# Optimization experiments

Measured on AMD Instinct MI355X. Metric: run time of the kernel, lower is better.

Reference implementation:

```python
import jax, jax.numpy as jnp
import numpy as np

N_NODES = 50000
N_EDGES = 1200000
IN_FEATS = 64
OUT_FEATS = 64
NEG_SLOPE = 0.01  # F.leaky_relu default


def setup_inputs() -> dict:
    key = jax.random.key(0)
    k1, k2, k3, k4, k5, k6 = jax.random.split(key, 6)
    feature = jax.random.normal(k1, (N_NODES, IN_FEATS), dtype=jnp.float32)
    attn_w = jax.random.normal(k2, (2 * IN_FEATS, 1), dtype=jnp.float32) * 0.1
    lin_w = jax.random.normal(k3, (OUT_FEATS, 2 * IN_FEATS), dtype=jnp.float32) * 0.1
    lin_b = jax.random.normal(k4, (OUT_FEATS,), dtype=jnp.float32) * 0.1
    src = jax.random.randint(k5, (N_EDGES,), 0, N_NODES, dtype=jnp.int32)
    dst = jax.random.randint(k6, (N_EDGES,), 0, N_NODES, dtype=jnp.int32)
    return {"feature": feature, "attn_w": attn_w, "lin_w": lin_w,
            "lin_b": lin_b, "src": src, "dst": dst}


def reference(feature, attn_w, lin_w, lin_b, src, dst):
    N = feature.shape[0]
    # edge attention: leaky_relu(attn_fc([h_src, h_dst]))
    # split attn weight to avoid materializing the [E, 2*in] concat
    a_src, a_dst = attn_w[:IN_FEATS, 0], attn_w[IN_FEATS:, 0]
    e = jax.nn.leaky_relu(feature[src] @ a_src + feature[dst] @ a_dst,
                          negative_slope=NEG_SLOPE)  # [E]
    # segment softmax over incoming edges of each destination node
    emax = jax.ops.segment_max(e, dst, num_segments=N)
    emax = jnp.where(jnp.isfinite(emax), emax, 0.0)  # guard empty segments
    ex = jnp.exp(e - emax[dst])                       # [E]
    denom = jax.ops.segment_sum(ex, dst, num_segments=N)          # [N]
    num = jax.ops.segment_sum(ex[:, None] * feature[src], dst,
                              num_segments=N)                      # [N, in]
    hm = jnp.where(denom[:, None] > 0, num / denom[:, None], 0.0)
    # node apply: relu(Linear([h, hm]))
    h = jnp.concatenate([feature, hm], axis=1) @ lin_w.T + lin_b
    return jax.nn.relu(h)
```

## Files before the change

### kernel.cpp

```cpp
#include <hip/hip_runtime.h>
#include <math.h>

#define N_NODES 50000
#define N_EDGES 1200000
#define F 64
#define CAP 49
#define OVF_MAX 1024
#define NBIN 782
#define BSTR 16
#define CAP_BIN 2304
#define TILE 8192
#define NTILE ((N_EDGES + TILE - 1) / TILE)

typedef __attribute__((ext_vector_type(8))) short short8;
typedef __attribute__((ext_vector_type(4))) float v4f;


__device__ __forceinline__ unsigned short f32_to_bf16_rne(float f) {
    unsigned u = __float_as_uint(f);
    return (unsigned short)((u + 0x7FFFu + ((u >> 16) & 1u)) >> 16);
}
__device__ __forceinline__ float bf16_to_f32(unsigned short u) {
    return __uint_as_float(((unsigned)u) << 16);
}

__global__ void k_prep(const float* __restrict__ feature,
                       const float* __restrict__ attn_w,
                       float* __restrict__ s, float* __restrict__ dd,
                       int* __restrict__ bin_cnt, int* __restrict__ ovf_cnt,
                       unsigned short* __restrict__ fb) {
    int gid = blockIdx.x * blockDim.x + threadIdx.x;
    if (gid < NBIN * BSTR) bin_cnt[gid] = 0;
    if (gid == NBIN * BSTR) *ovf_cnt = 0;
    int wave = gid >> 6;
    int lane = threadIdx.x & 63;
    if (wave >= N_NODES) return;
    float f = feature[wave * F + lane];
    fb[wave * F + lane] = f32_to_bf16_rne(f);
    float sv = f * attn_w[lane];
    float dv = f * attn_w[F + lane];
    #pragma unroll
    for (int o = 32; o > 0; o >>= 1) {
        sv += __shfl_down(sv, o, 64);
        dv += __shfl_down(dv, o, 64);
    }
    if (lane == 0) {
        s[wave] = sv;
        dd[wave] = dv;
    }
}

__global__ __launch_bounds__(256) void k_bin(
        const int* __restrict__ src, const int* __restrict__ dst,
        int* __restrict__ bin_cnt, unsigned* __restrict__ binned) {
    __shared__ unsigned ord[TILE];
    __shared__ int cnt_l[NBIN], off_l[NBIN], cur_l[NBIN], base_g[NBIN];
    __shared__ int buf[256];
    int t = threadIdx.x;
    int e0 = blockIdx.x * TILE;
    int ecnt = N_EDGES - e0; if (ecnt > TILE) ecnt = TILE;
    for (int i = t; i < NBIN; i += 256) cnt_l[i] = 0;
    __syncthreads();
    int n4 = ecnt >> 2;
    const int4* s4p = (const int4*)src + (e0 >> 2);
    const int4* d4p = (const int4*)dst + (e0 >> 2);
    for (int c = t; c < n4; c += 256) {
        int4 d4 = d4p[c];
        atomicAdd(&cnt_l[d4.x >> 6], 1);
        atomicAdd(&cnt_l[d4.y >> 6], 1);
        atomicAdd(&cnt_l[d4.z >> 6], 1);
        atomicAdd(&cnt_l[d4.w >> 6], 1);
    }
    __syncthreads();
    int c0[4];
    int sum = 0;
    #pragma unroll
    for (int j = 0; j < 4; j++) {
        int idx = t * 4 + j;
        c0[j] = (idx < NBIN) ? cnt_l[idx] : 0;
        sum += c0[j];
    }
    buf[t] = sum;
    __syncthreads();
    #pragma unroll
    for (int d = 1; d < 256; d <<= 1) {
        int x = (t >= d) ? buf[t - d] : 0;
        __syncthreads();
        buf[t] += x;
        __syncthreads();
    }
    int excl = buf[t] - sum;
    #pragma unroll
    for (int j = 0; j < 4; j++) {
        int idx = t * 4 + j;
        if (idx < NBIN) {
            off_l[idx] = excl;
            cur_l[idx] = excl;
            base_g[idx] = atomicAdd(&bin_cnt[idx * BSTR], c0[j]);
        }
        excl += c0[j];
    }
    __syncthreads();
    for (int c = t; c < n4; c += 256) {
        int4 d4 = d4p[c];
        int4 s4 = s4p[c];
        int dv[4] = {d4.x, d4.y, d4.z, d4.w};
        int sv[4] = {s4.x, s4.y, s4.z, s4.w};
        #pragma unroll
        for (int u = 0; u < 4; u++) {
            int r = atomicAdd(&cur_l[dv[u] >> 6], 1);
            ord[r] = (((unsigned)dv[u]) << 16) | (unsigned)sv[u];
        }
    }
    __syncthreads();
    for (int i = t; i < ecnt; i += 256) {
        unsigned v = ord[i];
        int b = v >> 22;
        int pos = base_g[b] + (i - off_l[b]);
        if (pos < CAP_BIN) binned[(size_t)b * CAP_BIN + pos] = v;
    }
}

__global__ __launch_bounds__(256) void k_fused(
        const unsigned* __restrict__ binned, const int* __restrict__ bin_cnt,
        int* __restrict__ cnt, unsigned short* __restrict__ bucket,
        int* __restrict__ ovf_cnt, unsigned* __restrict__ ovf,
        const float* __restrict__ s, const float* __restrict__ dd,
        const unsigned short* __restrict__ fb,
        const float* __restrict__ lin_w, const float* __restrict__ lin_b,
        float* __restrict__ out) {
    __shared__ int cnt_l[64];
    __shared__ unsigned short buck_l[64 * CAP];
    __shared__ unsigned short Wl[64 * 136];
    __shared__ float xl[4][16][64];
    int t = threadIdx.x;
    int wid = t >> 6, lane = t & 63;
    int bin = blockIdx.x;
    int n0 = bin << 6;
    int nn = N_NODES - n0; if (nn > 64) nn = 64;
    for (int i = t; i < 64 * 128; i += 256)
        Wl[(i >> 7) * 136 + (i & 127)] = f32_to_bf16_rne(lin_w[i]);
    if (t < 64) cnt_l[t] = 0;
    __syncthreads();
    int E = bin_cnt[bin * BSTR];
    if (E > CAP_BIN) E = CAP_BIN;
    const unsigned* be = binned + (size_t)bin * CAP_BIN;
    for (int i = t; i < E; i += 256) {
        unsigned v = be[i];
        int local = (v >> 16) & 63;
        int sid = (int)(v & 0xFFFFu);
        int r = atomicAdd(&cnt_l[local], 1);
        if (r < CAP) {
            buck_l[local * CAP + r] = (unsigned short)sid;
        } else {
            int o = atomicAdd(ovf_cnt, 1);
            if (o < OVF_MAX)
                ovf[o] = ((unsigned)(n0 + local) << 16) | (unsigned)sid;
        }
    }
    __syncthreads();
    if (t < nn) {
        cnt[n0 + t] = cnt_l[t];
        if (cnt_l[t] > CAP) {
            for (int k2 = 0; k2 < CAP; k2++)
                bucket[(size_t)(n0 + t) * CAP + k2] = buck_l[t * CAP + k2];
        }
    }
    __syncthreads();
    const ushort4* f4 = (const ushort4*)fb;
    for (int j = 0; j < 16; j++) {
        int local = wid * 16 + j;
        if (local >= nn) break;
        int deg = cnt_l[local];
        if (deg == 0 || deg > CAP) {
            if (lane < 16) {
                v4f z = {0.0f, 0.0f, 0.0f, 0.0f};
                ((v4f*)&xl[wid][j][0])[lane] = z;
            }
            continue;
        }
        int si = 0;
        float ev = -1e30f;
        if (lane < deg) {
            si = (int)buck_l[local * CAP + lane];
            float v = s[si] + dd[n0 + local];
            ev = v > 0.0f ? v : 0.01f * v;
        }
        float m = ev;
        #pragma unroll
        for (int o = 32; o > 0; o >>= 1)
            m = fmaxf(m, __shfl_xor(m, o, 64));
        float p = (lane < deg) ? __expf(ev - m) : 0.0f;
        float l = p;
        #pragma unroll
        for (int o = 32; o > 0; o >>= 1)
            l += __shfl_xor(l, o, 64);
        p *= __builtin_amdgcn_rcpf(l);
        int grp = lane >> 4;
        int c16 = lane & 15;
        ushort4 fv0[8], fv1[8];
        #pragma unroll
        for (int u = 0; u < 8; u++) {
            int sk = __shfl(si, u * 4 + grp, 64);
            fv0[u] = f4[sk * 16 + c16];
        }
        bool two = deg > 32;
        if (two) {
            #pragma unroll
            for (int u = 0; u < 8; u++) {
                int sk = __shfl(si, 32 + u * 4 + grp, 64);
                fv1[u] = f4[sk * 16 + c16];
            }
        }
        float a0 = 0.0f, a1 = 0.0f, a2 = 0.0f, a3 = 0.0f;
        #pragma unroll
        for (int u = 0; u < 8; u++) {
            float pw = __shfl(p, u * 4 + grp, 64);
            a0 = fmaf(pw, bf16_to_f32(fv0[u].x), a0);
            a1 = fmaf(pw, bf16_to_f32(fv0[u].y), a1);
            a2 = fmaf(pw, bf16_to_f32(fv0[u].z), a2);
            a3 = fmaf(pw, bf16_to_f32(fv0[u].w), a3);
        }
        if (two) {
            #pragma unroll
            for (int u = 0; u < 8; u++) {
                float pw = __shfl(p, 32 + u * 4 + grp, 64);
                a0 = fmaf(pw, bf16_to_f32(fv1[u].x), a0);
                a1 = fmaf(pw, bf16_to_f32(fv1[u].y), a1);
                a2 = fmaf(pw, bf16_to_f32(fv1[u].z), a2);
                a3 = fmaf(pw, bf16_to_f32(fv1[u].w), a3);
            }
        }
        a0 += __shfl_xor(a0, 16, 64); a0 += __shfl_xor(a0, 32, 64);
        a1 += __shfl_xor(a1, 16, 64); a1 += __shfl_xor(a1, 32, 64);
        a2 += __shfl_xor(a2, 16, 64); a2 += __shfl_xor(a2, 32, 64);
        a3 += __shfl_xor(a3, 16, 64); a3 += __shfl_xor(a3, 32, 64);
        if (lane < 16) {
            v4f st = {a0, a1, a2, a3};
            ((v4f*)&xl[wid][j][0])[c16] = st;
        }
    }
    int n0w = n0 + wid * 16;
    if (n0w >= N_NODES) return;
    int m = lane & 15, quad = lane >> 4;
    short8 afr[4];
    #pragma unroll
    for (int ks = 0; ks < 2; ks++) {
        int kb = ks * 32 + quad * 8;
        afr[ks] = *(const short8*)&fb[(size_t)(n0w + m) * F + kb];
    }
    #pragma unroll
    for (int ks = 2; ks < 4; ks++) {
        int kb = ks * 32 + quad * 8 - 64;
        const float* sp = &xl[wid][m][kb];
        float4 x0 = ((const float4*)sp)[0];
        float4 x1 = ((const float4*)sp)[1];
        short8 a;
        a[0] = (short)f32_to_bf16_rne(x0.x);
        a[1] = (short)f32_to_bf16_rne(x0.y);
        a[2] = (short)f32_to_bf16_rne(x0.z);
        a[3] = (short)f32_to_bf16_rne(x0.w);
        a[4] = (short)f32_to_bf16_rne(x1.x);
        a[5] = (short)f32_to_bf16_rne(x1.y);
        a[6] = (short)f32_to_bf16_rne(x1.z);
        a[7] = (short)f32_to_bf16_rne(x1.w);
        afr[ks] = a;
    }
    #pragma unroll
    for (int nt = 0; nt < 4; nt++) {
        v4f acc = {0.0f, 0.0f, 0.0f, 0.0f};
        #pragma unroll
        for (int ks = 0; ks < 4; ks++) {
            int kb = ks * 32 + quad * 8;
            short8 b = *(const short8*)&Wl[(nt * 16 + m) * 136 + kb];
            acc = __builtin_amdgcn_mfma_f32_16x16x32_bf16(afr[ks], b, acc,
                                                          0, 0, 0);
        }
        int colo = nt * 16 + m;
        float bias = lin_b[colo];
        #pragma unroll
        for (int r = 0; r < 4; r++) {
            int row = quad * 4 + r;
            float v = acc[r] + bias;
            out[(size_t)(n0w + row) * F + colo] = fmaxf(v, 0.0f);
        }
    }
}

__global__ __launch_bounds__(256) void k_cleanup(
        const unsigned short* __restrict__ bucket,
        const int* __restrict__ cnt,
        const int* __restrict__ ovf_cnt, const unsigned int* __restrict__ ovf,
        const float* __restrict__ s, const float* __restrict__ dd,
        const float* __restrict__ feature,
        const float* __restrict__ lin_w, const float* __restrict__ lin_b,
        float* __restrict__ out) {
    int M = *ovf_cnt;
    if (M > OVF_MAX) M = OVF_MAX;
    if (M == 0) return;
    __shared__ float Wl[64 * 129];
    __shared__ int list[128];
    __shared__ int nlist;
    __shared__ unsigned short edg[4][256];
    __shared__ float xc[4][128];
    int t = threadIdx.x;
    for (int i = t; i < 64 * 128; i += 256)
        Wl[(i >> 7) * 129 + (i & 127)] = lin_w[i];
    if (t == 0) {
        nlist = 0;
        for (int i = 0; i < M; i++) {
            int d = (int)(ovf[i] >> 16);
            bool seen = false;
            for (int j = 0; j < nlist; j++) if (list[j] == d) seen = true;
            if (!seen && nlist < 128) list[nlist++] = d;
        }
    }
    __syncthreads();
    int wid = t >> 6, lane = t & 63;
    for (int idx = wid; idx < nlist; idx += 4) {
        int n = list[idx];
        int deg = cnt[n];
        if (lane < CAP) edg[wid][lane] = bucket[n * CAP + lane];
        int k2 = CAP;
        for (int base = 0; base < M; base += 64) {
            int i2 = base + lane;
            unsigned val = 0;
            bool mt = false;
            if (i2 < M) { val = ovf[i2]; mt = ((int)(val >> 16) == n); }
            unsigned long long mask = __ballot(mt);
            if (mt) {
                int pos = k2 + __popcll(mask & ((1ULL << lane) - 1ULL));
                if (pos < 256) edg[wid][pos] = (unsigned short)(val & 0xFFFFu);
            }
            k2 += __popcll(mask);
        }
        __threadfence_block();
        int nd = deg < 256 ? deg : 256;
        float m = -1e30f, l = 0.0f, acc = 0.0f;
        float dn = dd[n];
        for (int c0 = 0; c0 < nd; c0 += 64) {
            int j = c0 + lane;
            int sid = 0;
            float ev = -1e30f;
            if (j < nd) {
                sid = (int)edg[wid][j];
                float v = s[sid] + dn;
                ev = v > 0.0f ? v : 0.01f * v;
            }
            float cm = ev;
            #pragma unroll
            for (int o = 32; o > 0; o >>= 1)
                cm = fmaxf(cm, __shfl_xor(cm, o, 64));
            float np = (j < nd) ? __expf(ev - cm) : 0.0f;
            float cl = np;
            #pragma unroll
            for (int o = 32; o > 0; o >>= 1)
                cl += __shfl_xor(cl, o, 64);
            float cacc = 0.0f;
            int c = nd - c0; if (c > 64) c = 64;
            for (int k = 0; k < c; k += 16) {
                float fvv[16];
                #pragma unroll
                for (int u = 0; u < 16; u++) {
                    int sk = __builtin_amdgcn_readlane(sid, k + u);
                    fvv[u] = feature[sk * F + lane];
                }
                #pragma unroll
                for (int u = 0; u < 16; u++) {
                    float pk = __uint_as_float(
                        __builtin_amdgcn_readlane(__float_as_uint(np), k + u));
                    cacc = fmaf(pk, fvv[u], cacc);
                }
            }
            float mn = fmaxf(m, cm);
            float sc = __expf(m - mn);
            float sc2 = __expf(cm - mn);
            l = l * sc + cl * sc2;
            acc = acc * sc + cacc * sc2;
            m = mn;
        }
        float hm = acc / l;
        xc[wid][lane] = feature[n * F + lane];
        xc[wid][64 + lane] = hm;
        __threadfence_block();
        float oa = lin_b[lane];
        #pragma unroll
        for (int k = 0; k < 128; k++)
            oa += xc[wid][k] * Wl[lane * 129 + k];
        out[n * F + lane] = fmaxf(oa, 0.0f);
    }
}

extern "C" void kernel_launch(void* const* d_in, const int* in_sizes, int n_in,
                              void* d_out, int out_size, void* d_ws, size_t ws_size,
                              hipStream_t stream) {
    const float* feature = (const float*)d_in[0];
    const float* attn_w  = (const float*)d_in[1];
    const float* lin_w   = (const float*)d_in[2];
    const float* lin_b   = (const float*)d_in[3];
    const int*   src     = (const int*)d_in[4];
    const int*   dst     = (const int*)d_in[5];
    float* out = (float*)d_out;
    char* ws = (char*)d_ws;

    float*          s       = (float*)(ws);
    float*          dd      = (float*)(ws + 200000);
    int*            cnt     = (int*)  (ws + 400000);
    int*            bin_cnt = (int*)  (ws + 600000);
    int*            ovf_cnt = (int*)  (ws + 650048);
    unsigned*       ovf     = (unsigned*)(ws + 650112);
    unsigned short* bucket  = (unsigned short*)(ws + 654208);
    unsigned*       binned  = (unsigned*)(ws + 5554208);
    unsigned short* fb      = (unsigned short*)(ws + 12761120);

    k_prep<<<(N_NODES * 64) / 256, 256, 0, stream>>>(
        feature, attn_w, s, dd, bin_cnt, ovf_cnt, fb);
    k_bin<<<NTILE, 256, 0, stream>>>(src, dst, bin_cnt, binned);
    k_fused<<<NBIN, 256, 0, stream>>>(
        binned, bin_cnt, cnt, bucket, ovf_cnt, ovf, s, dd, fb,
        lin_w, lin_b, out);
    k_cleanup<<<1, 256, 0, stream>>>(
        bucket, cnt, ovf_cnt, ovf, s, dd, feature, lin_w, lin_b, out);
}
```

Before: 143.1 us.

## Cache packed edges in registers during binning and shrink fused-kernel LDS with bf16 staging

In the binning kernel, each thread now loads src/dst once into a 32-entry register array of packed (dst<<16|src) words and reuses them for the scatter pass, instead of reading global memory twice. In the fused kernel, the aggregated-neighbor staging buffer is stored as bf16 with a padded stride rather than fp32, and launch bounds request 4 blocks per SM. The smaller staging buffer cuts LDS use, which can allow more resident blocks, and the MFMA A-fragment load becomes a direct short8 read. The per-thread register array in k_bin raises register pressure, and bf16 rounding now happens before the LDS store rather than after the read, which should give the same values.

```diff
diff --git a/kernel.cpp b/kernel.cpp
--- a/kernel.cpp
+++ b/kernel.cpp
@@ -11,6 +11,7 @@
 #define CAP_BIN 2304
 #define TILE 8192
 #define NTILE ((N_EDGES + TILE - 1) / TILE)
+#define XSTR 72
 
 typedef __attribute__((ext_vector_type(8))) short short8;
 typedef __attribute__((ext_vector_type(4))) float v4f;
@@ -64,12 +65,24 @@
     int n4 = ecnt >> 2;
     const int4* s4p = (const int4*)src + (e0 >> 2);
     const int4* d4p = (const int4*)dst + (e0 >> 2);
-    for (int c = t; c < n4; c += 256) {
-        int4 d4 = d4p[c];
-        atomicAdd(&cnt_l[d4.x >> 6], 1);
-        atomicAdd(&cnt_l[d4.y >> 6], 1);
-        atomicAdd(&cnt_l[d4.z >> 6], 1);
-        atomicAdd(&cnt_l[d4.w >> 6], 1);
+    unsigned pk[32];
+    int ng = 0;
+    #pragma unroll
+    for (int k = 0; k < 8; k++) {
+        int c = t + k * 256;
+        if (c < n4) {
+            int4 d4 = d4p[c];
+            int4 s4 = s4p[c];
+            pk[4 * k + 0] = (((unsigned)d4.x) << 16) | (unsigned)s4.x;
+            pk[4 * k + 1] = (((unsigned)d4.y) << 16) | (unsigned)s4.y;
+            pk[4 * k + 2] = (((unsigned)d4.z) << 16) | (unsigned)s4.z;
+            pk[4 * k + 3] = (((unsigned)d4.w) << 16) | (unsigned)s4.w;
+            atomicAdd(&cnt_l[pk[4 * k + 0] >> 22], 1);
+            atomicAdd(&cnt_l[pk[4 * k + 1] >> 22], 1);
+            atomicAdd(&cnt_l[pk[4 * k + 2] >> 22], 1);
+            atomicAdd(&cnt_l[pk[4 * k + 3] >> 22], 1);
+            ng = k + 1;
+        }
     }
     __syncthreads();
     int c0[4];
@@ -101,15 +114,12 @@
         excl += c0[j];
     }
     __syncthreads();
-    for (int c = t; c < n4; c += 256) {
-        int4 d4 = d4p[c];
-        int4 s4 = s4p[c];
-        int dv[4] = {d4.x, d4.y, d4.z, d4.w};
-        int sv[4] = {s4.x, s4.y, s4.z, s4.w};
+    for (int k = 0; k < ng; k++) {
         #pragma unroll
         for (int u = 0; u < 4; u++) {
-            int r = atomicAdd(&cur_l[dv[u] >> 6], 1);
-            ord[r] = (((unsigned)dv[u]) << 16) | (unsigned)sv[u];
+            unsigned v = pk[4 * k + u];
+            int r = atomicAdd(&cur_l[v >> 22], 1);
+            ord[r] = v;
         }
     }
     __syncthreads();
@@ -121,7 +131,7 @@
     }
 }
 
-__global__ __launch_bounds__(256) void k_fused(
+__global__ __launch_bounds__(256, 4) void k_fused(
         const unsigned* __restrict__ binned, const int* __restrict__ bin_cnt,
         int* __restrict__ cnt, unsigned short* __restrict__ bucket,
         int* __restrict__ ovf_cnt, unsigned* __restrict__ ovf,
@@ -132,7 +142,7 @@
     __shared__ int cnt_l[64];
     __shared__ unsigned short buck_l[64 * CAP];
     __shared__ unsigned short Wl[64 * 136];
-    __shared__ float xl[4][16][64];
+    __shared__ __align__(16) unsigned short xl[4][16][XSTR];
     int t = threadIdx.x;
     int wid = t >> 6, lane = t & 63;
     int bin = blockIdx.x;
@@ -174,8 +184,8 @@
         int deg = cnt_l[local];
         if (deg == 0 || deg > CAP) {
             if (lane < 16) {
-                v4f z = {0.0f, 0.0f, 0.0f, 0.0f};
-                ((v4f*)&xl[wid][j][0])[lane] = z;
+                ushort4 z = {0, 0, 0, 0};
+                *(ushort4*)&xl[wid][j][lane * 4] = z;
             }
             continue;
         }
@@ -236,8 +246,12 @@
         a2 += __shfl_xor(a2, 16, 64); a2 += __shfl_xor(a2, 32, 64);
         a3 += __shfl_xor(a3, 16, 64); a3 += __shfl_xor(a3, 32, 64);
         if (lane < 16) {
-            v4f st = {a0, a1, a2, a3};
-            ((v4f*)&xl[wid][j][0])[c16] = st;
+            ushort4 st;
+            st.x = f32_to_bf16_rne(a0);
+            st.y = f32_to_bf16_rne(a1);
+            st.z = f32_to_bf16_rne(a2);
+            st.w = f32_to_bf16_rne(a3);
+            *(ushort4*)&xl[wid][j][c16 * 4] = st;
         }
     }
     int n0w = n0 + wid * 16;
@@ -251,20 +265,8 @@
     }
     #pragma unroll
     for (int ks = 2; ks < 4; ks++) {
-        int kb = ks * 32 + quad * 8 - 64;
-        const float* sp = &xl[wid][m][kb];
-        float4 x0 = ((const float4*)sp)[0];
-        float4 x1 = ((const float4*)sp)[1];
-        short8 a;
-        a[0] = (short)f32_to_bf16_rne(x0.x);
-        a[1] = (short)f32_to_bf16_rne(x0.y);
-        a[2] = (short)f32_to_bf16_rne(x0.z);
-        a[3] = (short)f32_to_bf16_rne(x0.w);
-        a[4] = (short)f32_to_bf16_rne(x1.x);
-        a[5] = (short)f32_to_bf16_rne(x1.y);
-        a[6] = (short)f32_to_bf16_rne(x1.z);
-        a[7] = (short)f32_to_bf16_rne(x1.w);
-        afr[ks] = a;
+        int kb = (ks - 2) * 32 + quad * 8;
+        afr[ks] = *(const short8*)&xl[wid][m][kb];
     }
     #pragma unroll
     for (int nt = 0; nt < 4; nt++) {
```

Result: no change. 141.9 us (-0.9%).
